# Optimization experiments

Hardware: AMD Instinct MI355X
Metric: run time of the kernel (lower is better)

## Reference

```python
import jax, jax.numpy as jnp
from jax import lax
import numpy as np

B, A, T = 128, 32, 32
HID = 64
DEG = 7
MODES = 25
OUT_FRAMES = 12
NHEAD, DHEAD = 16, 64


def legendre_tmat(out_frames, degree):
    # normalized Legendre basis evaluated at t_n, shape [degree+1, len(t_n)]
    t = np.arange(-6, out_frames + 1, dtype=np.float32)
    t = t / t[-1]
    P = [np.ones_like(t), t]
    for n in range(1, degree):
        P.append(((2 * n + 1) * t * P[n] - n * P[n - 1]) / (n + 1))
    P = np.stack(P[: degree + 1], 0)
    norm = np.sqrt((2 * np.arange(degree + 1) + 1) / 2.0).astype(np.float32)
    return (P * norm[:, None]).astype(np.float32)


def _conv(x, w, stride, pad):
    return lax.conv_general_dilated(x, w, (stride, stride), [(pad, pad), (pad, pad)],
                                    dimension_numbers=("NCHW", "OIHW", "NCHW"))


def _bn(x, g, b, eps=1e-5):
    m = jnp.mean(x, axis=(0, 2, 3), keepdims=True)
    v = jnp.var(x, axis=(0, 2, 3), keepdims=True)
    return (x - m) / jnp.sqrt(v + eps) * g[None, :, None, None] + b[None, :, None, None]


def setup_inputs() -> dict:
    key = jax.random.key(0)
    ks = jax.random.split(key, 32)

    def rn(i, shape, scale=0.05):
        return jax.random.normal(ks[i], shape, dtype=jnp.float32) * scale

    inp = {
        "cnn_feat": rn(0, (B, 1024, 14, 14), 1.0),
        "ego_state": rn(1, (B, T, 5), 1.0),
        "agents_state": rn(2, (B, A, T, 5), 1.0),
        "ego_state_len": jax.random.randint(ks[3], (B,), 0, T),
        "agents_state_len": jax.random.randint(ks[4], (B, A), 0, T),
        "agents_grid_pos": jax.random.randint(ks[5], (B, A, 2), 0, 14),
        "state_fc_W": rn(6, (HID, 5)), "state_fc_b": rn(7, (HID,)),
        "lstm_Wih": rn(8, (4 * HID, HID)), "lstm_Whh": rn(9, (4 * HID, HID)),
        "lstm_bih": rn(10, (4 * HID,)), "lstm_bhh": rn(11, (4 * HID,)),
        "enc_fc_W": rn(12, (HID, HID)), "enc_fc_b": rn(13, (HID,)),
        "conv1_W": rn(14, (512, 1024 + HID, 3, 3)),
        "bn1_g": jnp.ones((512,), jnp.float32), "bn1_b": jnp.zeros((512,), jnp.float32),
        "conv2_W": rn(15, (512, 512, 3, 3)),
        "bn2_g": jnp.ones((512,), jnp.float32), "bn2_b": jnp.zeros((512,), jnp.float32),
        "q_W": rn(16, (NHEAD * DHEAD, 512 + HID)),
        "k_W": rn(17, (NHEAD * DHEAD, 512, 1, 1)),
        "v_W": rn(18, (NHEAD * DHEAD, 512, 1, 1)),
        "attn_out_W": rn(19, (512, NHEAD * DHEAD)), "attn_out_b": rn(20, (512,)),
        "cls_W": rn(21, (MODES, 512 + HID + 512)), "cls_b": rn(22, (MODES,)),
        "dec1_W": rn(23, (256, 512 + HID + 512)), "dec1_b": rn(24, (256,)),
        "dec2_W": rn(25, ((DEG + 1) * 2 * MODES, 256)), "dec2_b": rn(26, ((DEG + 1) * 2 * MODES,)),
    }
    return inp


def reference(cnn_feat, ego_state, agents_state, ego_state_len, agents_state_len,
              agents_grid_pos, state_fc_W, state_fc_b, lstm_Wih, lstm_Whh, lstm_bih,
              lstm_bhh, enc_fc_W, enc_fc_b, conv1_W, bn1_g, bn1_b, conv2_W, bn2_g,
              bn2_b, q_W, k_W, v_W, attn_out_W, attn_out_b, cls_W, cls_b, dec1_W,
              dec1_b, dec2_W, dec2_b):
    Bn, _, Hs, Ws = cnn_feat.shape

    def lstm_encode(seq, lens):
        # seq [N,T,5]; packed-sequence semantics with zero init == take h at step len-1
        N, Tn, _ = seq.shape
        h = seq @ state_fc_W.T + state_fc_b  # [N,T,64]

        def step(carry, xt):
            hh, cc = carry
            g = xt @ lstm_Wih.T + hh @ lstm_Whh.T + lstm_bih + lstm_bhh
            i, f_, gg, o = jnp.split(g, 4, axis=-1)
            cc = jax.nn.sigmoid(f_) * cc + jax.nn.sigmoid(i) * jnp.tanh(gg)
            hh = jax.nn.sigmoid(o) * jnp.tanh(cc)
            return (hh, cc), hh

        z = jnp.zeros((N, HID), h.dtype)
        _, hs = lax.scan(step, (z, z), h.transpose(1, 0, 2))  # hs [T,N,64]
        idx = jnp.clip(lens, 1, Tn).astype(jnp.int32) - 1
        last = hs[idx, jnp.arange(N)]
        return last @ enc_fc_W.T + enc_fc_b

    ego = lstm_encode(ego_state, ego_state_len)  # [B,64]
    ag = lstm_encode(agents_state.reshape(Bn * A, T, 5),
                     agents_state_len.reshape(-1)).reshape(Bn, A, HID)

    # scatter-add agent encodings into the spatial grid (overlapping writes accumulate)
    grid = jnp.zeros((Bn, Hs, Ws, HID), cnn_feat.dtype)
    bidx = jnp.broadcast_to(jnp.arange(Bn)[:, None], (Bn, A))
    grid = grid.at[bidx, agents_grid_pos[..., 0], agents_grid_pos[..., 1]].add(ag)

    x = jnp.concatenate([cnn_feat, grid.transpose(0, 3, 1, 2)], axis=1)
    x = jax.nn.relu(_bn(_conv(x, conv1_W, 1, 1), bn1_g, bn1_b))
    x = jax.nn.relu(_bn(_conv(x, conv2_W, 2, 1), bn2_g, bn2_b))  # [B,512,7,7]

    ego_t = jnp.concatenate([x[:, :, 3, 3], ego], axis=1)  # [B,576]
    q = (ego_t @ q_W.T).reshape(Bn, NHEAD, DHEAD)
    k = _conv(x, k_W, 1, 1).reshape(Bn, NHEAD, DHEAD, -1)  # g = 9*9 = 81
    v = _conv(x, v_W, 1, 1).reshape(Bn, NHEAD, DHEAD, -1)
    energy = jnp.einsum("bhf,bhfg->bhg", q, k)
    attn = jax.nn.softmax(energy / (NHEAD * DHEAD) ** 0.5, axis=2)
    o = jnp.einsum("bhg,bhdg->bhd", attn, v).reshape(Bn, -1)
    o = o @ attn_out_W.T + attn_out_b

    feat = jnp.concatenate([o, ego_t], axis=1)  # [B,1088]
    conf = feat @ cls_W.T + cls_b
    d = jax.nn.relu(feat @ dec1_W.T + dec1_b)
    d = (d @ dec2_W.T + dec2_b).reshape(Bn, MODES, -1)

    tmat = jnp.asarray(legendre_tmat(OUT_FRAMES, DEG))  # [DEG+1, 19]
    out_x = d[:, :, : DEG + 1] @ tmat
    out_y = d[:, :, DEG + 1:] @ tmat
    traj = jnp.stack([out_x, out_y], axis=3)  # [B,MODES,19,2]
    return traj, conf
```

## Files before the change

### kernel.cpp

```cpp
#include <hip/hip_runtime.h>
#include <stdint.h>
#include <stddef.h>

#define DEVINL static __device__ __forceinline__

typedef __attribute__((ext_vector_type(8))) short  bfrag;
typedef __attribute__((ext_vector_type(4))) float  facc;

DEVINL uint16_t f2b(float f){
  uint32_t u = __float_as_uint(f);
  return (uint16_t)((u + 0x7fffu + ((u >> 16) & 1u)) >> 16);
}
DEVINL float b2f(uint16_t b){ return __uint_as_float(((uint32_t)b) << 16); }

DEVINL facc MFMA(bfrag a, bfrag b, facc c){
  return __builtin_amdgcn_mfma_f32_16x16x32_bf16(a, b, c, 0, 0, 0);
}

DEVINL void gload16(const void* g, void* l){
  __builtin_amdgcn_global_load_lds(
      (const __attribute__((address_space(1))) uint32_t*)g,
      (__attribute__((address_space(3))) uint32_t*)l, 16, 0, 0);
}

DEVINL float fast_tanh(float x){
  return 2.f/(1.f+__expf(-2.f*x)) - 1.f;
}

struct F2BJobs {
  const float* s[7];
  uint16_t*    d[7];
  int          n[7];
};
__global__ void k_f2b_multi(F2BJobs jobs){
  int j = blockIdx.y;
  const float* s = jobs.s[j];
  uint16_t* d = jobs.d[j];
  int n = jobs.n[j];
  int i = blockIdx.x*256 + threadIdx.x;
  int st = gridDim.x*256;
  for(; i<n; i+=st) d[i] = f2b(s[i]);
}

__global__ void k_zborder(uint16_t* __restrict__ X, int C){
  int b = blockIdx.x, t = threadIdx.x;
  for(int p=0;p<60;p++){
    int y, x;
    if(p<16){ y=0; x=p; }
    else if(p<32){ y=15; x=p-16; }
    else { int q=p-32; y=1+(q>>1); x=(q&1)?15:0; }
    uint32_t* dst = (uint32_t*)(X + ((size_t)(b*16+y)*16 + x)*C);
    for(int i=t;i<C/2;i+=256) dst[i] = 0;
  }
}

__global__ void k_lstm_prep(const float* __restrict__ Wih, const float* __restrict__ Whh,
                            const float* __restrict__ bih, const float* __restrict__ bhh,
                            const float* __restrict__ sW, const float* __restrict__ sb,
                            const float* __restrict__ encW,
                            uint16_t* __restrict__ Wc, float* __restrict__ be,
                            uint16_t* __restrict__ encWb, float* __restrict__ tm){
  int n = threadIdx.x;
  if(n < 19){
    float tv = (float)(n - 6) / 12.0f;
    float Pm = 1.0f, Pc = tv;
    tm[0*19+n] = Pm * sqrtf(0.5f);
    tm[1*19+n] = Pc * sqrtf(1.5f);
    for(int q=1; q<7; q++){
      float Pn = ((float)(2*q+1)*tv*Pc - (float)q*Pm) / (float)(q+1);
      Pm = Pc; Pc = Pn;
      tm[(q+1)*19+n] = Pc * sqrtf((float)(2*(q+1)+1) * 0.5f);
    }
  }
  for(int k=0;k<64;k++) Wc[n*96+k] = f2b(Whh[n*64+k]);
  for(int k5=0;k5<5;k5++){
    float s = 0.f;
    for(int j=0;j<64;j++) s += Wih[n*64+j]*sW[j*5+k5];
    Wc[n*96+64+k5] = f2b(s);
  }
  for(int k=69;k<96;k++) Wc[n*96+k] = 0;
  float s = 0.f;
  for(int j=0;j<64;j++) s += Wih[n*64+j]*sb[j];
  be[n] = s + bih[n] + bhh[n];
  if(n < 64){
    for(int k=0;k<64;k++) encWb[n*64+k] = f2b(encW[n*64+k]);
  }
}

__global__ __launch_bounds__(256) void k_lstm(
    const float* __restrict__ ego_seq, const float* __restrict__ ag_seq,
    const int* __restrict__ ego_len, const int* __restrict__ ag_len,
    const int* __restrict__ grid_pos,
    const uint16_t* __restrict__ Wc, const float* __restrict__ be,
    const uint16_t* __restrict__ encWb, const float* __restrict__ encB,
    float* __restrict__ agrid, uint16_t* __restrict__ egoT, uint16_t* __restrict__ feat)
{
  __shared__ __align__(16) uint16_t A[32*96];
  __shared__ float Xf[32*160];
  __shared__ int   idxs[32];

  int t = threadIdx.x, w = t>>6, l = t&63;
  int blk = blockIdx.x;
  bool isEgo = blk < 4;
  int seq0 = isEgo ? blk*32 : (blk-4)*32;
  const float* seqp = (isEgo ? ego_seq : ag_seq) + (size_t)seq0*160;

  for(int i=t;i<32*160;i+=256) Xf[i] = seqp[i];
  if(t < 32){
    int L = isEgo ? ego_len[seq0+t] : ag_len[seq0+t];
    if(L < 1) L = 1;
    idxs[t] = L-1;
  }
  for(int i=t;i<32*96;i+=256) A[i] = 0;

  bfrag bf[4][3];
  float be4[4];
  for(int ct=0;ct<4;ct++){
    int n = (ct*4+w)*16 + (l&15);
    for(int ks=0;ks<3;ks++)
      bf[ct][ks] = *(const bfrag*)(Wc + n*96 + ks*32 + (l>>4)*8);
    be4[ct] = be[n];
  }
  float cst[8], hl[8];
  for(int i=0;i<8;i++){ cst[i]=0.f; hl[i]=0.f; }
  __syncthreads();
  int myidx[8];
  for(int rt=0;rt<2;rt++) for(int r=0;r<4;r++){
    int s = rt*16 + (l>>4)*4 + r;
    myidx[rt*4+r] = idxs[s];
  }

  for(int st=0; st<32; st++){
    if(t < 160){ int s=t/5, kk=t%5; A[s*96+64+kk] = f2b(Xf[s*160 + st*5 + kk]); }
    __syncthreads();
    facc acc[2][4];
    for(int rt=0;rt<2;rt++) for(int ct=0;ct<4;ct++) acc[rt][ct] = facc{0.f,0.f,0.f,0.f};
    #pragma unroll
    for(int ks=0;ks<3;ks++){
      bfrag aA[2];
      #pragma unroll
      for(int rt=0;rt<2;rt++)
        aA[rt] = *(const bfrag*)(A + (rt*16+(l&15))*96 + ks*32 + (l>>4)*8);
      #pragma unroll
      for(int rt=0;rt<2;rt++)
        #pragma unroll
        for(int ct=0;ct<4;ct++)
          acc[rt][ct] = MFMA(aA[rt], bf[ct][ks], acc[rt][ct]);
    }
    __syncthreads();
    #pragma unroll
    for(int rt=0;rt<2;rt++) for(int r=0;r<4;r++){
      int cell = rt*4+r;
      int s = rt*16 + (l>>4)*4 + r;
      float gi = acc[rt][0][r] + be4[0];
      float gf = acc[rt][1][r] + be4[1];
      float gg = acc[rt][2][r] + be4[2];
      float go = acc[rt][3][r] + be4[3];
      float si = 1.f/(1.f+__expf(-gi));
      float sf = 1.f/(1.f+__expf(-gf));
      float so = 1.f/(1.f+__expf(-go));
      float tg = fast_tanh(gg);
      float c2 = sf*cst[cell] + si*tg;
      cst[cell] = c2;
      float hn = so*fast_tanh(c2);
      A[s*96 + w*16 + (l&15)] = f2b(hn);
      if(st == myidx[cell]) hl[cell] = hn;
    }
  }
  __syncthreads();
  for(int rt=0;rt<2;rt++) for(int r=0;r<4;r++){
    int s = rt*16 + (l>>4)*4 + r;
    A[s*96 + w*16 + (l&15)] = f2b(hl[rt*4+r]);
  }
  __syncthreads();
  bfrag eb[2];
  for(int ks=0;ks<2;ks++)
    eb[ks] = *(const bfrag*)(encWb + (w*16+(l&15))*64 + ks*32 + (l>>4)*8);
  facc ea[2]; ea[0] = facc{0.f,0.f,0.f,0.f}; ea[1] = facc{0.f,0.f,0.f,0.f};
  for(int ks=0;ks<2;ks++){
    for(int rt=0;rt<2;rt++){
      bfrag aA = *(const bfrag*)(A + (rt*16+(l&15))*96 + ks*32 + (l>>4)*8);
      ea[rt] = MFMA(aA, eb[ks], ea[rt]);
    }
  }
  int n = w*16 + (l&15);
  float bn_ = encB[n];
  for(int rt=0;rt<2;rt++) for(int r=0;r<4;r++){
    int s = rt*16 + (l>>4)*4 + r;
    float v = ea[rt][r] + bn_;
    int gs = seq0 + s;
    if(isEgo){
      egoT[(size_t)gs*576 + 512 + n] = f2b(v);
      feat[(size_t)gs*1088 + 1024 + n] = f2b(v);
    } else {
      int py = grid_pos[gs*2+0], px = grid_pos[gs*2+1];
      atomicAdd(&agrid[((size_t)(gs>>5)*196 + py*14 + px)*64 + n], v);
    }
  }
}

__global__ void k_packx(const float* __restrict__ cnn, const float* __restrict__ agrid,
                        uint16_t* __restrict__ Xp)
{
  __shared__ float tile[32*200];
  int b = blockIdx.x, ch = blockIdx.y, t = threadIdx.x;
  if(ch < 32){
    int c0 = ch*32;
    for(int i=t;i<32*196;i+=256){
      int ci = i/196, s = i%196;
      tile[ci*200+s] = cnn[((size_t)b*1024 + c0+ci)*196 + s];
    }
    __syncthreads();
    for(int i=t;i<32*196;i+=256){
      int s = i>>5, ci = i&31;
      int y = s/14, x = s%14;
      Xp[(((size_t)b*16 + y+1)*16 + x+1)*1088 + c0 + ci] = f2b(tile[ci*200+s]);
    }
  } else {
    int j0 = (ch-32)*32;
    for(int i=t;i<32*196;i+=256){
      int s = i>>5, ji = i&31;
      int y = s/14, x = s%14;
      Xp[(((size_t)b*16 + y+1)*16 + x+1)*1088 + 1024 + j0 + ji] =
          f2b(agrid[((size_t)b*196 + s)*64 + j0 + ji]);
    }
  }
}

__global__ void k_packw(const float* __restrict__ W, uint16_t* __restrict__ Wp, int O, int C)
{
  int o = blockIdx.x;
  int c = blockIdx.y*64 + threadIdx.x;
  const float* src = W + ((size_t)o*C + c)*9;
  float v[9];
  #pragma unroll
  for(int d=0;d<9;d++) v[d] = src[d];
  #pragma unroll
  for(int d=0;d<9;d++)
    Wp[((size_t)d*O + o)*C + c] = f2b(v[d]);
}

__global__ __launch_bounds__(512) void k_conv1_8p(
    const uint16_t* __restrict__ Ain, const uint16_t* __restrict__ Wb,
    uint16_t* __restrict__ Out, float* __restrict__ stats)
{
  constexpr int CB = 1088;
  constexpr int NSTEP = 153;
  __shared__ __align__(16) char LDSb[131072];

  int t = threadIdx.x, w = t>>6, l = t&63;
  int wm = w>>2, wn = w&3;

  int xcd = blockIdx.x & 7, pos = blockIdx.x >> 3;
  int wgid = (xcd < 4 ? xcd*25 : 100 + (xcd-4)*24) + pos;
  int m0 = (wgid % 98) * 256;
  int n0 = (wgid / 98) * 256;

  const uint16_t* aP[2][2];
  const uint16_t* bP[2][2];
  #pragma unroll
  for(int P=0;P<2;P++)
    #pragma unroll
    for(int j=0;j<2;j++){
      int partrow = j*64 + (t>>3);
      int swz = ((t&7) ^ (partrow&7))*8;
      int gr = P*64 + partrow + ((partrow>=64)?64:0);
      int m = m0 + gr; int b = m/196, s = m%196, y = s/14, x = s%14;
      aP[P][j] = Ain + ((b*16+y)*16+x)*CB + swz;
      int nb = n0 + (partrow>>5)*64 + P*32 + (partrow&31);
      bP[P][j] = Wb + (size_t)nb*CB + swz;
    }

  facc acc[8][4];
  #pragma unroll
  for(int i=0;i<8;i++)
    #pragma unroll
    for(int j=0;j<4;j++) acc[i][j] = facc{0.f,0.f,0.f,0.f};

  int dd = 0;

  #define STG(buf, PART) do{                                                   \
    if((PART)==0 || (PART)==3){ const int P_ = ((PART)==3);                    \
      _Pragma("unroll")                                                        \
      for(int j_=0;j_<2;j_++)                                                  \
        gload16(aP[P_][j_], LDSb + (buf)*65536 + P_*16384 + j_*8192 + w*1024); \
    } else { const int P_ = ((PART)==2);                                       \
      _Pragma("unroll")                                                        \
      for(int j_=0;j_<2;j_++)                                                  \
        gload16(bP[P_][j_], LDSb + (buf)*65536 + 32768 + P_*16384 + j_*8192 + w*1024); \
    }                                                                          \
  }while(0)

  #define ADVK() do{                                                          \
    if(dd==8){                                                                \
      _Pragma("unroll")                                                       \
      for(int P_=0;P_<2;P_++) for(int j_=0;j_<2;j_++){                        \
        aP[P_][j_] += 64 - 34*CB; bP[P_][j_] += 64 - 8*512*CB; }              \
      dd = 0;                                                                 \
    } else {                                                                  \
      int sA_ = (dd==2||dd==5) ? 14*CB : CB;                                  \
      _Pragma("unroll")                                                       \
      for(int P_=0;P_<2;P_++) for(int j_=0;j_<2;j_++){                        \
        aP[P_][j_] += sA_; bP[P_][j_] += 512*CB; }                            \
      dd++;                                                                   \
    }                                                                         \
  }while(0)

  #define VM4 asm volatile("s_waitcnt vmcnt(4)" ::: "memory")
  #define VM2 asm volatile("s_waitcnt vmcnt(2)" ::: "memory")
  #define VM0 asm volatile("s_waitcnt vmcnt(0)" ::: "memory")

  #define PHASE(mh, nh, SP, DO_STG, WAIT) do{                                 \
    const uint16_t* Ab_ = (const uint16_t*)(LDSb + p*65536 + (mh)*16384);     \
    const uint16_t* Bb_ = (const uint16_t*)(LDSb + p*65536 + 32768 + (nh)*16384); \
    bfrag a_[4][2], b_[2][2];                                                 \
    _Pragma("unroll")                                                         \
    for(int i_=0;i_<4;i_++)                                                   \
      _Pragma("unroll")                                                       \
      for(int ks_=0;ks_<2;ks_++)                                              \
        a_[i_][ks_] = *(const bfrag*)(Ab_ + (wm*64 + i_*16 + (l&15))*64       \
                        + ((ks_*32 + (l>>4)*8) ^ ((l&7)<<3)));                \
    _Pragma("unroll")                                                         \
    for(int j_=0;j_<2;j_++)                                                   \
      _Pragma("unroll")                                                       \
      for(int ks_=0;ks_<2;ks_++)                                              \
        b_[j_][ks_] = *(const bfrag*)(Bb_ + (wn*32 + j_*16 + (l&15))*64       \
                        + ((ks_*32 + (l>>4)*8) ^ ((l&7)<<3)));                \
    if(DO_STG) STG(p^1, SP);                                                  \
    __builtin_amdgcn_sched_barrier(0);                                        \
    __builtin_amdgcn_s_barrier();                                             \
    __builtin_amdgcn_s_setprio(1);                                            \
    _Pragma("unroll")                                                         \
    for(int ks_=0;ks_<2;ks_++)                                                \
      _Pragma("unroll")                                                       \
      for(int i_=0;i_<4;i_++)                                                 \
        _Pragma("unroll")                                                     \
        for(int j_=0;j_<2;j_++)                                               \
          acc[(mh)*4+i_][(nh)*2+j_] =                                         \
            MFMA(a_[i_][ks_], b_[j_][ks_], acc[(mh)*4+i_][(nh)*2+j_]);        \
    __builtin_amdgcn_s_setprio(0);                                            \
    WAIT;                                                                     \
    __builtin_amdgcn_s_barrier();                                             \
  }while(0)

  STG(0,0); STG(0,1); STG(0,2); STG(0,3);
  ADVK();
  VM4;
  __builtin_amdgcn_s_barrier();

  for(int kt=0; kt<NSTEP-1; kt++){
    int p = kt&1;
    PHASE(0,0, 0, 1, VM4);
    PHASE(0,1, 1, 1, VM4);
    PHASE(1,0, 2, 1, (void)0);
    PHASE(1,1, 3, 1, VM4);
    if(kt < NSTEP-2) ADVK();
  }
  {
    int p = 0;
    PHASE(0,0, 0, 0, VM2);
    PHASE(0,1, 1, 0, VM0);
    PHASE(1,0, 2, 0, (void)0);
    PHASE(1,1, 3, 0, (void)0);
  }

  #undef PHASE
  #undef STG
  #undef ADVK

  __syncthreads();
  int* oo = (int*)LDSb;
  if(t < 256){
    int m = m0 + t; int b = m/196, s = m%196, y = s/14, x = s%14;
    oo[t] = ((b*16 + y+1)*16 + (x+1))*512;
  }
  __syncthreads();
  #pragma unroll
  for(int i=0;i<8;i++)
    #pragma unroll
    for(int j=0;j<4;j++){
      int n = n0 + wn*64 + j*16 + (l&15);
      #pragma unroll
      for(int r=0;r<4;r++){
        int mr = wm*128 + i*16 + (l>>4)*4 + r;
        Out[(size_t)oo[mr] + n] = f2b(acc[i][j][r]);
      }
    }
  __syncthreads();
  float* sred = (float*)LDSb;
  int rg = wm*4 + (l>>4);
  #pragma unroll
  for(int j=0;j<4;j++){
    float s=0.f, q=0.f;
    #pragma unroll
    for(int i=0;i<8;i++)
      #pragma unroll
      for(int r=0;r<4;r++){ float v = acc[i][j][r]; s += v; q += v*v; }
    int nl = wn*64 + j*16 + (l&15);
    sred[(nl*8 + rg)*2+0] = s;
    sred[(nl*8 + rg)*2+1] = q;
  }
  __syncthreads();
  if(t < 256){
    float s=0.f, q=0.f;
    #pragma unroll
    for(int rgi=0;rgi<8;rgi++){ s += sred[(t*8+rgi)*2]; q += sred[(t*8+rgi)*2+1]; }
    atomicAdd(&stats[n0+t], s);
    atomicAdd(&stats[512+n0+t], q);
  }
}

template<int MODE>
__global__ __launch_bounds__(256) void k_conv(
    const uint16_t* __restrict__ Ain, const uint16_t* __restrict__ Wb,
    uint16_t* __restrict__ Out, float* __restrict__ stats)
{
  constexpr int CB   = 512;
  constexpr int NB   = (MODE==2) ? 2048 : 512;
  constexpr int NDY  = (MODE==2) ? 1 : 9;
  constexpr int NCC  = 8;
  constexpr int MT   = 49;
  constexpr int NT   = NB/128;
  constexpr int NWG  = MT*NT;
  constexpr int Q8   = NWG/8, R8 = NWG%8;

  __shared__ __align__(16) uint16_t As[128*64];
  __shared__ __align__(16) uint16_t Bs[128*64];
  __shared__ int outOff[128];

  int t = threadIdx.x, w = t>>6, l = t&63;

  int xcd = blockIdx.x & 7, pos = blockIdx.x >> 3;
  int wgid = (xcd < R8 ? xcd*(Q8+1) : R8*(Q8+1) + (xcd-R8)*Q8) + pos;
  int n0 = (wgid / MT) * 128;
  int m0 = (wgid % MT) * 128;

  if(t < 128){
    int m = m0 + t;
    outOff[t] = (MODE==1) ? m*512 : m*2048;
  }

  const uint16_t* aP[4];
  const uint16_t* bP[4];
  #pragma unroll
  for(int p=0;p<4;p++){
    int r = w*32 + p*8 + (l>>3);
    int m = m0 + r, ro;
    if(MODE==1){
      int b = m/49, s = m%49, y = s/7, x = s%7;
      ro = ((b*16 + 2*y)*16 + 2*x)*512;
    } else {
      ro = m*512;
    }
    aP[p] = Ain + ro + (l&7)*8;
    bP[p] = Wb + (size_t)(n0 + r)*CB + (l&7)*8;
  }
  __syncthreads();

  facc acc[4][4];
  #pragma unroll
  for(int i=0;i<4;i++)
    #pragma unroll
    for(int j=0;j<4;j++) acc[i][j] = facc{0.f,0.f,0.f,0.f};
  int wm = w>>1, wn = w&1;
  char* asDst = (char*)As + w*4096;
  char* bsDst = (char*)Bs + w*4096;

  for(int cc=0; cc<NCC; cc++){
    for(int d=0; d<NDY; d++){
      #pragma unroll
      for(int p=0;p<4;p++) gload16(aP[p], asDst + p*1024);
      #pragma unroll
      for(int p=0;p<4;p++) gload16(bP[p], bsDst + p*1024);
      if(MODE != 2){
        int stepA = ((d%3)==2) ? 14*CB : CB;
        #pragma unroll
        for(int p=0;p<4;p++){ aP[p] += stepA; bP[p] += NB*CB; }
      }
      __syncthreads();
      #pragma unroll
      for(int ks=0;ks<2;ks++){
        bfrag a[4], b[4];
        #pragma unroll
        for(int i=0;i<4;i++)
          a[i] = *(const bfrag*)(As + (wm*64 + i*16 + (l&15))*64 + ks*32 + (l>>4)*8);
        #pragma unroll
        for(int j=0;j<4;j++)
          b[j] = *(const bfrag*)(Bs + (wn*64 + j*16 + (l&15))*64 + ks*32 + (l>>4)*8);
        #pragma unroll
        for(int i=0;i<4;i++)
          #pragma unroll
          for(int j=0;j<4;j++)
            acc[i][j] = MFMA(a[i], b[j], acc[i][j]);
      }
      __syncthreads();
    }
    int resetA = (MODE==2) ? 64 : 64 - 48*CB;
    int resetB = (MODE==2) ? 64 : 64 - 9*NB*CB;
    #pragma unroll
    for(int p=0;p<4;p++){ aP[p] += resetA; bP[p] += resetB; }
  }

  #pragma unroll
  for(int i=0;i<4;i++)
    #pragma unroll
    for(int j=0;j<4;j++){
      int n = n0 + wn*64 + j*16 + (l&15);
      #pragma unroll
      for(int r=0;r<4;r++){
        int mr = wm*64 + i*16 + (l>>4)*4 + r;
        Out[(size_t)outOff[mr] + n] = f2b(acc[i][j][r]);
      }
    }

  if(MODE != 2){
    __syncthreads();
    float* sred = (float*)As;
    int rg = wm*4 + (l>>4);
    #pragma unroll
    for(int j=0;j<4;j++){
      float s=0.f, q=0.f;
      #pragma unroll
      for(int i=0;i<4;i++)
        #pragma unroll
        for(int r=0;r<4;r++){ float v = acc[i][j][r]; s += v; q += v*v; }
      int nl = wn*64 + j*16 + (l&15);
      sred[(nl*8 + rg)*2+0] = s;
      sred[(nl*8 + rg)*2+1] = q;
    }
    __syncthreads();
    if(t < 128){
      float s=0.f, q=0.f;
      #pragma unroll
      for(int rgi=0;rgi<8;rgi++){ s += sred[(t*8+rgi)*2]; q += sred[(t*8+rgi)*2+1]; }
      atomicAdd(&stats[n0+t], s);
      atomicAdd(&stats[512+n0+t], q);
    }
  }
}

template<int PAD>
__global__ void k_bnapply(uint16_t* __restrict__ Y, const float* __restrict__ stats,
                          const float* __restrict__ gg, const float* __restrict__ bb,
                          int M, float invM,
                          uint16_t* __restrict__ egoT, uint16_t* __restrict__ feat)
{
  int t = threadIdx.x;
  int m0 = blockIdx.x*8;
  float mu0 = stats[2*t]*invM,       mu1 = stats[2*t+1]*invM;
  float v0 = stats[512+2*t]*invM - mu0*mu0, v1 = stats[512+2*t+1]*invM - mu1*mu1;
  float sc0 = gg[2*t]  *rsqrtf(v0+1e-5f), sc1 = gg[2*t+1]*rsqrtf(v1+1e-5f);
  float sh0 = bb[2*t]   - mu0*sc0,        sh1 = bb[2*t+1] - mu1*sc1;
  for(int i=0;i<8;i++){
    int m = m0+i; if(m>=M) break;
    size_t off;
    if(PAD){ int b=m/196, s=m%196, y=s/14, x=s%14; off = (((size_t)b*16+y+1)*16 + x+1)*512; }
    else off = (size_t)m*512;
    uint32_t u = *(const uint32_t*)(Y + off + 2*t);
    float a = fmaxf(b2f((uint16_t)u)*sc0 + sh0, 0.f);
    float c = fmaxf(b2f((uint16_t)(u>>16))*sc1 + sh1, 0.f);
    uint32_t pu = (uint32_t)f2b(a) | ((uint32_t)f2b(c)<<16);
    *(uint32_t*)(Y + off + 2*t) = pu;
    if(!PAD && (m%49)==24){
      int b = m/49;
      *(uint32_t*)(egoT + (size_t)b*576 + 2*t) = pu;
      *(uint32_t*)(feat + (size_t)b*1088 + 512 + 2*t) = pu;
    }
  }
}

__global__ __launch_bounds__(256) void k_sgemm(
    const uint16_t* __restrict__ A, int lda,
    const uint16_t* __restrict__ B, int ldb,
    const float* __restrict__ bias,
    void* __restrict__ C, int ldc,
    int N, int K, int flags)
{
  int t = threadIdx.x, w = t>>6, l = t&63;
  int nt = blockIdx.x*4 + w;
  int n  = nt*16 + (l&15);
  int m0 = blockIdx.y*16;
  bool nv = n < N;
  facc acc = facc{0.f,0.f,0.f,0.f};
  for(int k=0;k<K;k+=32){
    bfrag af = *(const bfrag*)(A + (size_t)(m0+(l&15))*lda + k + (l>>4)*8);
    bfrag bf_ = {0,0,0,0,0,0,0,0};
    if(nv) bf_ = *(const bfrag*)(B + (size_t)n*ldb + k + (l>>4)*8);
    acc = MFMA(af, bf_, acc);
  }
  if(nv){
    float bv = bias ? bias[n] : 0.f;
    #pragma unroll
    for(int r=0;r<4;r++){
      int m = m0 + (l>>4)*4 + r;
      float v = acc[r] + bv;
      if(flags & 1) v = fmaxf(v, 0.f);
      if(flags & 2) ((float*)C)[(size_t)m*ldc + n] = v;
      else ((uint16_t*)C)[(size_t)m*ldc + n] = f2b(v);
    }
  }
}

__global__ __launch_bounds__(256) void k_attn(
    const float* __restrict__ q, const uint16_t* __restrict__ kv,
    uint16_t* __restrict__ o)
{
  int t = threadIdx.x, w = t>>6, l = t&63;
  int idx = blockIdx.x*4 + w;
  int b = idx>>4, h = idx&15;
  float qf = q[(size_t)b*1024 + h*64 + l];
  const uint16_t* kp = kv + (size_t)b*49*2048 + h*64 + l;
  float eo = 0.f;
  for(int g=0; g<49; g++){
    float p = qf * b2f(kp[(size_t)g*2048]);
    for(int s=32;s>0;s>>=1) p += __shfl_xor(p, s);
    if(l == g) eo = p;
  }
  float e = (l<49) ? eo*(1.f/32.f) : -1e30f;
  float mx = e;
  for(int s=32;s>0;s>>=1) mx = fmaxf(mx, __shfl_xor(mx, s));
  mx = fmaxf(mx, 0.f);
  float p = (l<49) ? __expf(e-mx) : 0.f;
  float den = p;
  for(int s=32;s>0;s>>=1) den += __shfl_xor(den, s);
  den += 32.f*__expf(-mx);
  const uint16_t* vp = kv + (size_t)b*49*2048 + 1024 + h*64 + l;
  float accv = 0.f;
  for(int g=0; g<49; g++){
    float pg = __shfl(p, g);
    accv += pg * b2f(vp[(size_t)g*2048]);
  }
  o[(size_t)b*1024 + h*64 + l] = f2b(accv/den);
}

__global__ void k_traj(const float* __restrict__ d2, const float* __restrict__ tm,
                       float* __restrict__ out)
{
  int i = blockIdx.x*256 + threadIdx.x;
  if(i >= 3200) return;
  const float* dp = d2 + (size_t)i*16;
  float cx[8], cy[8];
  #pragma unroll
  for(int j=0;j<8;j++){ cx[j]=dp[j]; cy[j]=dp[8+j]; }
  float* op = out + (size_t)i*38;
  for(int tt=0;tt<19;tt++){
    float x=0.f, y=0.f;
    #pragma unroll
    for(int j=0;j<8;j++){ float tv = tm[j*19+tt]; x += cx[j]*tv; y += cy[j]*tv; }
    op[tt*2+0]=x; op[tt*2+1]=y;
  }
}

extern "C" void kernel_launch(void* const* d_in, const int* in_sizes, int n_in,
                              void* d_out, int out_size, void* d_ws, size_t ws_size,
                              hipStream_t stream)
{
  const float* cnn      = (const float*)d_in[0];
  const float* ego_seq  = (const float*)d_in[1];
  const float* ag_seq   = (const float*)d_in[2];
  const int*   ego_len  = (const int*)d_in[3];
  const int*   ag_len   = (const int*)d_in[4];
  const int*   grid_pos = (const int*)d_in[5];
  const float* sW  = (const float*)d_in[6];
  const float* sb  = (const float*)d_in[7];
  const float* Wih = (const float*)d_in[8];
  const float* Whh = (const float*)d_in[9];
  const float* bih = (const float*)d_in[10];
  const float* bhh = (const float*)d_in[11];
  const float* encW = (const float*)d_in[12];
  const float* encB = (const float*)d_in[13];
  const float* conv1W = (const float*)d_in[14];
  const float* bn1g = (const float*)d_in[15];
  const float* bn1b = (const float*)d_in[16];
  const float* conv2W = (const float*)d_in[17];
  const float* bn2g = (const float*)d_in[18];
  const float* bn2b = (const float*)d_in[19];
  const float* qWf  = (const float*)d_in[20];
  const float* kWf  = (const float*)d_in[21];
  const float* vWf  = (const float*)d_in[22];
  const float* aoW  = (const float*)d_in[23];
  const float* aoB  = (const float*)d_in[24];
  const float* clsWf = (const float*)d_in[25];
  const float* clsB  = (const float*)d_in[26];
  const float* d1Wf  = (const float*)d_in[27];
  const float* d1B   = (const float*)d_in[28];
  const float* d2Wf  = (const float*)d_in[29];
  const float* d2B   = (const float*)d_in[30];

  char* ws = (char*)d_ws;
  const size_t XP_OFF   = 0;
  const size_t KV_OFF   = 0;
  const size_t Y2_OFF   = 29360128;
  const size_t Y1P_OFF  = 71303168;
  const size_t WP1_OFF  = 104857600;
  const size_t WP2_OFF  = 114884608;
  const size_t WKV_OFF  = 119603200;
  const size_t QW_OFF   = 121700352;
  const size_t AOW_OFF  = 122880000;
  const size_t CLSW_OFF = 123928576;
  const size_t D1W_OFF  = 123982976;
  const size_t D2W_OFF  = 124540032;
  const size_t GRID_OFF = 124744832;
  const size_t EGOT_OFF = 131167360;
  const size_t FEAT_OFF = 131314816;
  const size_t QBUF_OFF = 131593344;
  const size_t OBUF_OFF = 132117632;
  const size_t D1_OFF   = 132379776;
  const size_t D2_OFF   = 132445312;
  const size_t WC_OFF   = 132650112;
  const size_t BE_OFF   = 132699264;
  const size_t ENCW_OFF = 132700288;
  const size_t TMAT_OFF = 132708480;
  const size_t ST1_OFF  = 132709120;
  const size_t ST2_OFF  = 132713216;

  uint16_t* XP   = (uint16_t*)(ws + XP_OFF);
  uint16_t* KV   = (uint16_t*)(ws + KV_OFF);
  uint16_t* Y2   = (uint16_t*)(ws + Y2_OFF);
  uint16_t* Y1P  = (uint16_t*)(ws + Y1P_OFF);
  uint16_t* WP1  = (uint16_t*)(ws + WP1_OFF);
  uint16_t* WP2  = (uint16_t*)(ws + WP2_OFF);
  uint16_t* WKV  = (uint16_t*)(ws + WKV_OFF);
  uint16_t* QW   = (uint16_t*)(ws + QW_OFF);
  uint16_t* AOW  = (uint16_t*)(ws + AOW_OFF);
  uint16_t* CLSW = (uint16_t*)(ws + CLSW_OFF);
  uint16_t* D1W  = (uint16_t*)(ws + D1W_OFF);
  uint16_t* D2W  = (uint16_t*)(ws + D2W_OFF);
  float*    GRIDB= (float*)(ws + GRID_OFF);
  uint16_t* EGOT = (uint16_t*)(ws + EGOT_OFF);
  uint16_t* FEAT = (uint16_t*)(ws + FEAT_OFF);
  float*    QBUF = (float*)(ws + QBUF_OFF);
  uint16_t* OBUF = (uint16_t*)(ws + OBUF_OFF);
  uint16_t* D1B  = (uint16_t*)(ws + D1_OFF);
  float*    D2B  = (float*)(ws + D2_OFF);
  uint16_t* WC   = (uint16_t*)(ws + WC_OFF);
  float*    BE   = (float*)(ws + BE_OFF);
  uint16_t* ENCWB= (uint16_t*)(ws + ENCW_OFF);
  float*    TMAT = (float*)(ws + TMAT_OFF);
  float*    ST1  = (float*)(ws + ST1_OFF);
  float*    ST2  = (float*)(ws + ST2_OFF);
  float*    outF = (float*)d_out;

  (void)hipMemsetAsync(ws + GRID_OFF, 0, 6422528, stream);
  (void)hipMemsetAsync(ws + ST1_OFF,  0, 8192, stream);

  k_zborder<<<128,256,0,stream>>>(XP, 1088);
  k_zborder<<<128,256,0,stream>>>(Y1P, 512);

  k_lstm_prep<<<1,256,0,stream>>>(Wih,Whh,bih,bhh,sW,sb,encW, WC,BE,ENCWB, TMAT);
  k_packw<<<dim3(512,17),64,0,stream>>>(conv1W, WP1, 512, 1088);
  k_packw<<<dim3(512,8), 64,0,stream>>>(conv2W, WP2, 512, 512);
  {
    F2BJobs jb;
    jb.s[0]=kWf;  jb.d[0]=WKV;              jb.n[0]=1024*512;
    jb.s[1]=vWf;  jb.d[1]=WKV + 1024*512;   jb.n[1]=1024*512;
    jb.s[2]=qWf;  jb.d[2]=QW;               jb.n[2]=1024*576;
    jb.s[3]=aoW;  jb.d[3]=AOW;              jb.n[3]=512*1024;
    jb.s[4]=clsWf;jb.d[4]=CLSW;             jb.n[4]=25*1088;
    jb.s[5]=d1Wf; jb.d[5]=D1W;              jb.n[5]=256*1088;
    jb.s[6]=d2Wf; jb.d[6]=D2W;              jb.n[6]=400*256;
    k_f2b_multi<<<dim3(48,7),256,0,stream>>>(jb);
  }

  k_lstm<<<132,256,0,stream>>>(ego_seq, ag_seq, ego_len, ag_len, grid_pos,
                               WC, BE, ENCWB, encB, GRIDB, EGOT, FEAT);
  k_packx<<<dim3(128,34),256,0,stream>>>(cnn, GRIDB, XP);
  k_conv1_8p<<<196,512,0,stream>>>(XP, WP1, Y1P, ST1);
  k_bnapply<1><<<3136,256,0,stream>>>(Y1P, ST1, bn1g, bn1b, 25088, 1.f/25088.f, nullptr, nullptr);
  k_conv<1><<<196,256,0,stream>>>(Y1P, WP2, Y2, ST2);
  k_bnapply<0><<<784,256,0,stream>>>(Y2, ST2, bn2g, bn2b, 6272, 1.f/6272.f, EGOT, FEAT);
  k_conv<2><<<784,256,0,stream>>>(Y2, WKV, KV, nullptr);
  k_sgemm<<<dim3(16,8),256,0,stream>>>(EGOT, 576, QW, 576, nullptr, QBUF, 1024, 1024, 576, 2);
  k_attn<<<512,256,0,stream>>>(QBUF, KV, OBUF);
  k_sgemm<<<dim3(8,8),256,0,stream>>>(OBUF, 1024, AOW, 1024, aoB, FEAT, 1088, 512, 1024, 0);
  k_sgemm<<<dim3(1,8),256,0,stream>>>(FEAT, 1088, CLSW, 1088, clsB, outF + 121600, 25, 25, 1088, 2);
  k_sgemm<<<dim3(4,8),256,0,stream>>>(FEAT, 1088, D1W, 1088, d1B, D1B, 256, 256, 1088, 1);
  k_sgemm<<<dim3(7,8),256,0,stream>>>(D1B, 256, D2W, 256, d2B, D2B, 400, 400, 256, 2);
  k_traj<<<13,256,0,stream>>>(D2B, TMAT, outF);

  (void)in_sizes; (void)n_in; (void)out_size; (void)ws_size;
}
```

Measured before the change: 677.0 us.

## Split conv2 over kernel rows into fp32 partials, reduce with BN stats

The stride-2 conv2 is split along its kernel-row dimension (dy) across a second grid axis, so each workgroup covers one row of three taps over a 1536-long K. This triples the workgroup count from 196 to 588 to fill more CUs. It adds a separate reduction kernel that sums the three fp32 partial planes, writes bf16 Y2 and accumulates BN statistics. The conv2 weights are repacked into a per-dy contiguous layout, the two border-zeroing launches are merged into one, and the KV 1x1 conv becomes its own specialized kernel. The cost is extra global traffic for roughly 38 MB of fp32 partials plus one more launch.

New measurement: 664.3 us. Within noise of the previous version (-1.9%).

```diff
diff --git a/kernel.cpp b/kernel.cpp
--- a/kernel.cpp
+++ b/kernel.cpp
@@ -42,14 +42,16 @@
   for(; i<n; i+=st) d[i] = f2b(s[i]);
 }
 
-__global__ void k_zborder(uint16_t* __restrict__ X, int C){
-  int b = blockIdx.x, t = threadIdx.x;
+__global__ void k_zborder(uint16_t* __restrict__ X, uint16_t* __restrict__ Y){
+  int b = blockIdx.x & 127, t = threadIdx.x;
+  uint16_t* base = (blockIdx.x < 128) ? X : Y;
+  int C = (blockIdx.x < 128) ? 1088 : 512;
   for(int p=0;p<60;p++){
     int y, x;
     if(p<16){ y=0; x=p; }
     else if(p<32){ y=15; x=p-16; }
     else { int q=p-32; y=1+(q>>1); x=(q&1)?15:0; }
-    uint32_t* dst = (uint32_t*)(X + ((size_t)(b*16+y)*16 + x)*C);
+    uint32_t* dst = (uint32_t*)(base + ((size_t)(b*16+y)*16 + x)*C);
     for(int i=t;i<C/2;i+=256) dst[i] = 0;
   }
 }
@@ -238,6 +240,21 @@
   #pragma unroll
   for(int d=0;d<9;d++)
     Wp[((size_t)d*O + o)*C + c] = f2b(v[d]);
+}
+
+__global__ void k_packw2(const float* __restrict__ W, uint16_t* __restrict__ Wp)
+{
+  int o = blockIdx.x;
+  int c = blockIdx.y*64 + threadIdx.x;
+  const float* src = W + ((size_t)o*512 + c)*9;
+  float v[9];
+  #pragma unroll
+  for(int d=0;d<9;d++) v[d] = src[d];
+  #pragma unroll
+  for(int dy=0;dy<3;dy++)
+    #pragma unroll
+    for(int dx=0;dx<3;dx++)
+      Wp[((size_t)(dy*512 + o))*1536 + dx*512 + c] = f2b(v[dy*3+dx]);
 }
 
 __global__ __launch_bounds__(512) void k_conv1_8p(
@@ -410,52 +427,31 @@
   }
 }
 
-template<int MODE>
-__global__ __launch_bounds__(256) void k_conv(
+__global__ __launch_bounds__(256) void k_conv2dy(
     const uint16_t* __restrict__ Ain, const uint16_t* __restrict__ Wb,
-    uint16_t* __restrict__ Out, float* __restrict__ stats)
-{
-  constexpr int CB   = 512;
-  constexpr int NB   = (MODE==2) ? 2048 : 512;
-  constexpr int NDY  = (MODE==2) ? 1 : 9;
-  constexpr int NCC  = 8;
-  constexpr int MT   = 49;
-  constexpr int NT   = NB/128;
-  constexpr int NWG  = MT*NT;
-  constexpr int Q8   = NWG/8, R8 = NWG%8;
-
+    float* __restrict__ PS)
+{
   __shared__ __align__(16) uint16_t As[128*64];
   __shared__ __align__(16) uint16_t Bs[128*64];
-  __shared__ int outOff[128];
 
   int t = threadIdx.x, w = t>>6, l = t&63;
+  int dy = blockIdx.y;
 
   int xcd = blockIdx.x & 7, pos = blockIdx.x >> 3;
-  int wgid = (xcd < R8 ? xcd*(Q8+1) : R8*(Q8+1) + (xcd-R8)*Q8) + pos;
-  int n0 = (wgid / MT) * 128;
-  int m0 = (wgid % MT) * 128;
-
-  if(t < 128){
-    int m = m0 + t;
-    outOff[t] = (MODE==1) ? m*512 : m*2048;
-  }
+  int wgid = (xcd < 4 ? xcd*25 : 100 + (xcd-4)*24) + pos;
+  int n0 = (wgid / 49) * 128;
+  int m0 = (wgid % 49) * 128;
 
   const uint16_t* aP[4];
   const uint16_t* bP[4];
   #pragma unroll
   for(int p=0;p<4;p++){
     int r = w*32 + p*8 + (l>>3);
-    int m = m0 + r, ro;
-    if(MODE==1){
-      int b = m/49, s = m%49, y = s/7, x = s%7;
-      ro = ((b*16 + 2*y)*16 + 2*x)*512;
-    } else {
-      ro = m*512;
-    }
-    aP[p] = Ain + ro + (l&7)*8;
-    bP[p] = Wb + (size_t)(n0 + r)*CB + (l&7)*8;
-  }
-  __syncthreads();
+    int m = m0 + r;
+    int b = m/49, s = m%49, y = s/7, x = s%7;
+    aP[p] = Ain + ((b*16 + 2*y + dy)*16 + 2*x)*512 + (l&7)*8;
+    bP[p] = Wb + ((size_t)(dy*512 + n0 + r))*1536 + (l&7)*8;
+  }
 
   facc acc[4][4];
   #pragma unroll
@@ -466,41 +462,31 @@
   char* asDst = (char*)As + w*4096;
   char* bsDst = (char*)Bs + w*4096;
 
-  for(int cc=0; cc<NCC; cc++){
-    for(int d=0; d<NDY; d++){
-      #pragma unroll
-      for(int p=0;p<4;p++) gload16(aP[p], asDst + p*1024);
-      #pragma unroll
-      for(int p=0;p<4;p++) gload16(bP[p], bsDst + p*1024);
-      if(MODE != 2){
-        int stepA = ((d%3)==2) ? 14*CB : CB;
-        #pragma unroll
-        for(int p=0;p<4;p++){ aP[p] += stepA; bP[p] += NB*CB; }
-      }
-      __syncthreads();
-      #pragma unroll
-      for(int ks=0;ks<2;ks++){
-        bfrag a[4], b[4];
-        #pragma unroll
-        for(int i=0;i<4;i++)
-          a[i] = *(const bfrag*)(As + (wm*64 + i*16 + (l&15))*64 + ks*32 + (l>>4)*8);
+  for(int stp=0; stp<24; stp++){
+    #pragma unroll
+    for(int p=0;p<4;p++){ gload16(aP[p], asDst + p*1024); aP[p] += 64; }
+    #pragma unroll
+    for(int p=0;p<4;p++){ gload16(bP[p], bsDst + p*1024); bP[p] += 64; }
+    __syncthreads();
+    #pragma unroll
+    for(int ks=0;ks<2;ks++){
+      bfrag a[4], b[4];
+      #pragma unroll
+      for(int i=0;i<4;i++)
+        a[i] = *(const bfrag*)(As + (wm*64 + i*16 + (l&15))*64 + ks*32 + (l>>4)*8);
+      #pragma unroll
+      for(int j=0;j<4;j++)
+        b[j] = *(const bfrag*)(Bs + (wn*64 + j*16 + (l&15))*64 + ks*32 + (l>>4)*8);
+      #pragma unroll
+      for(int i=0;i<4;i++)
         #pragma unroll
         for(int j=0;j<4;j++)
-          b[j] = *(const bfrag*)(Bs + (wn*64 + j*16 + (l&15))*64 + ks*32 + (l>>4)*8);
-        #pragma unroll
-        for(int i=0;i<4;i++)
-          #pragma unroll
-          for(int j=0;j<4;j++)
-            acc[i][j] = MFMA(a[i], b[j], acc[i][j]);
-      }
-      __syncthreads();
-    }
-    int resetA = (MODE==2) ? 64 : 64 - 48*CB;
-    int resetB = (MODE==2) ? 64 : 64 - 9*NB*CB;
-    #pragma unroll
-    for(int p=0;p<4;p++){ aP[p] += resetA; bP[p] += resetB; }
-  }
-
+          acc[i][j] = MFMA(a[i], b[j], acc[i][j]);
+    }
+    __syncthreads();
+  }
+
+  float* out = PS + (size_t)dy*3211264;
   #pragma unroll
   for(int i=0;i<4;i++)
     #pragma unroll
@@ -508,35 +494,105 @@
       int n = n0 + wn*64 + j*16 + (l&15);
       #pragma unroll
       for(int r=0;r<4;r++){
-        int mr = wm*64 + i*16 + (l>>4)*4 + r;
-        Out[(size_t)outOff[mr] + n] = f2b(acc[i][j][r]);
+        int mr = m0 + wm*64 + i*16 + (l>>4)*4 + r;
+        out[(size_t)mr*512 + n] = acc[i][j][r];
       }
     }
-
-  if(MODE != 2){
+}
+
+__global__ void k_bn2sum(const float* __restrict__ PS, uint16_t* __restrict__ Y2,
+                         float* __restrict__ stats)
+{
+  int t = threadIdx.x;
+  int m0 = blockIdx.x*128;
+  float s0=0,s1=0,q0=0,q1=0;
+  for(int i=0;i<128;i++){
+    size_t off = (size_t)(m0+i)*512 + 2*t;
+    float2 p0 = *(const float2*)(PS + off);
+    float2 p1 = *(const float2*)(PS + 3211264 + off);
+    float2 p2 = *(const float2*)(PS + 6422528 + off);
+    float a = p0.x+p1.x+p2.x, c = p0.y+p1.y+p2.y;
+    s0+=a; q0+=a*a; s1+=c; q1+=c*c;
+    *(uint32_t*)(Y2 + off) = (uint32_t)f2b(a) | ((uint32_t)f2b(c)<<16);
+  }
+  atomicAdd(&stats[2*t],   s0);
+  atomicAdd(&stats[2*t+1], s1);
+  atomicAdd(&stats[512+2*t],   q0);
+  atomicAdd(&stats[512+2*t+1], q1);
+}
+
+__global__ __launch_bounds__(256) void k_convkv(
+    const uint16_t* __restrict__ Ain, const uint16_t* __restrict__ Wb,
+    uint16_t* __restrict__ Out)
+{
+  constexpr int CB = 512;
+  constexpr int NB = 2048;
+  constexpr int NWG = 49*16;
+  constexpr int Q8 = NWG/8;
+
+  __shared__ __align__(16) uint16_t As[128*64];
+  __shared__ __align__(16) uint16_t Bs[128*64];
+
+  int t = threadIdx.x, w = t>>6, l = t&63;
+
+  int xcd = blockIdx.x & 7, pos = blockIdx.x >> 3;
+  int wgid = xcd*Q8 + pos;
+  int n0 = (wgid / 49) * 128;
+  int m0 = (wgid % 49) * 128;
+
+  const uint16_t* aP[4];
+  const uint16_t* bP[4];
+  #pragma unroll
+  for(int p=0;p<4;p++){
+    int r = w*32 + p*8 + (l>>3);
+    aP[p] = Ain + (size_t)(m0 + r)*512 + (l&7)*8;
+    bP[p] = Wb + (size_t)(n0 + r)*CB + (l&7)*8;
+  }
+
+  facc acc[4][4];
+  #pragma unroll
+  for(int i=0;i<4;i++)
+    #pragma unroll
+    for(int j=0;j<4;j++) acc[i][j] = facc{0.f,0.f,0.f,0.f};
+  int wm = w>>1, wn = w&1;
+  char* asDst = (char*)As + w*4096;
+  char* bsDst = (char*)Bs + w*4096;
+
+  for(int cc=0; cc<8; cc++){
+    #pragma unroll
+    for(int p=0;p<4;p++){ gload16(aP[p], asDst + p*1024); aP[p] += 64; }
+    #pragma unroll
+    for(int p=0;p<4;p++){ gload16(bP[p], bsDst + p*1024); bP[p] += 64; }
     __syncthreads();
-    float* sred = (float*)As;
-    int rg = wm*4 + (l>>4);
-    #pragma unroll
-    for(int j=0;j<4;j++){
-      float s=0.f, q=0.f;
+    #pragma unroll
+    for(int ks=0;ks<2;ks++){
+      bfrag a[4], b[4];
+      #pragma unroll
+      for(int i=0;i<4;i++)
+        a[i] = *(const bfrag*)(As + (wm*64 + i*16 + (l&15))*64 + ks*32 + (l>>4)*8);
+      #pragma unroll
+      for(int j=0;j<4;j++)
+        b[j] = *(const bfrag*)(Bs + (wn*64 + j*16 + (l&15))*64 + ks*32 + (l>>4)*8);
       #pragma unroll
       for(int i=0;i<4;i++)
         #pragma unroll
-        for(int r=0;r<4;r++){ float v = acc[i][j][r]; s += v; q += v*v; }
-      int nl = wn*64 + j*16 + (l&15);
-      sred[(nl*8 + rg)*2+0] = s;
-      sred[(nl*8 + rg)*2+1] = q;
+        for(int j=0;j<4;j++)
+          acc[i][j] = MFMA(a[i], b[j], acc[i][j]);
     }
     __syncthreads();
-    if(t < 128){
-      float s=0.f, q=0.f;
-      #pragma unroll
-      for(int rgi=0;rgi<8;rgi++){ s += sred[(t*8+rgi)*2]; q += sred[(t*8+rgi)*2+1]; }
-      atomicAdd(&stats[n0+t], s);
-      atomicAdd(&stats[512+n0+t], q);
-    }
-  }
+  }
+
+  #pragma unroll
+  for(int i=0;i<4;i++)
+    #pragma unroll
+    for(int j=0;j<4;j++){
+      int n = n0 + wn*64 + j*16 + (l&15);
+      #pragma unroll
+      for(int r=0;r<4;r++){
+        int mr = m0 + wm*64 + i*16 + (l>>4)*4 + r;
+        Out[(size_t)mr*2048 + n] = f2b(acc[i][j][r]);
+      }
+    }
 }
 
 template<int PAD>
@@ -689,8 +745,9 @@
 
   char* ws = (char*)d_ws;
   const size_t XP_OFF   = 0;
+  const size_t PS_OFF   = 0;
   const size_t KV_OFF   = 0;
-  const size_t Y2_OFF   = 29360128;
+  const size_t Y2_OFF   = 41943040;
   const size_t Y1P_OFF  = 71303168;
   const size_t WP1_OFF  = 104857600;
   const size_t WP2_OFF  = 114884608;
@@ -715,6 +772,7 @@
   const size_t ST2_OFF  = 132713216;
 
   uint16_t* XP   = (uint16_t*)(ws + XP_OFF);
+  float*    PS   = (float*)(ws + PS_OFF);
   uint16_t* KV   = (uint16_t*)(ws + KV_OFF);
   uint16_t* Y2   = (uint16_t*)(ws + Y2_OFF);
   uint16_t* Y1P  = (uint16_t*)(ws + Y1P_OFF);
@@ -744,12 +802,11 @@
   (void)hipMemsetAsync(ws + GRID_OFF, 0, 6422528, stream);
   (void)hipMemsetAsync(ws + ST1_OFF,  0, 8192, stream);
 
-  k_zborder<<<128,256,0,stream>>>(XP, 1088);
-  k_zborder<<<128,256,0,stream>>>(Y1P, 512);
+  k_zborder<<<256,256,0,stream>>>(XP, Y1P);
 
   k_lstm_prep<<<1,256,0,stream>>>(Wih,Whh,bih,bhh,sW,sb,encW, WC,BE,ENCWB, TMAT);
   k_packw<<<dim3(512,17),64,0,stream>>>(conv1W, WP1, 512, 1088);
-  k_packw<<<dim3(512,8), 64,0,stream>>>(conv2W, WP2, 512, 512);
+  k_packw2<<<dim3(512,8),64,0,stream>>>(conv2W, WP2);
   {
     F2BJobs jb;
     jb.s[0]=kWf;  jb.d[0]=WKV;              jb.n[0]=1024*512;
@@ -767,9 +824,10 @@
   k_packx<<<dim3(128,34),256,0,stream>>>(cnn, GRIDB, XP);
   k_conv1_8p<<<196,512,0,stream>>>(XP, WP1, Y1P, ST1);
   k_bnapply<1><<<3136,256,0,stream>>>(Y1P, ST1, bn1g, bn1b, 25088, 1.f/25088.f, nullptr, nullptr);
-  k_conv<1><<<196,256,0,stream>>>(Y1P, WP2, Y2, ST2);
+  k_conv2dy<<<dim3(196,3),256,0,stream>>>(Y1P, WP2, PS);
+  k_bn2sum<<<49,256,0,stream>>>(PS, Y2, ST2);
   k_bnapply<0><<<784,256,0,stream>>>(Y2, ST2, bn2g, bn2b, 6272, 1.f/6272.f, EGOT, FEAT);
-  k_conv<2><<<784,256,0,stream>>>(Y2, WKV, KV, nullptr);
+  k_convkv<<<784,256,0,stream>>>(Y2, WKV, KV);
   k_sgemm<<<dim3(16,8),256,0,stream>>>(EGOT, 576, QW, 576, nullptr, QBUF, 1024, 1024, 576, 2);
   k_attn<<<512,256,0,stream>>>(QBUF, KV, OBUF);
   k_sgemm<<<dim3(8,8),256,0,stream>>>(OBUF, 1024, AOW, 1024, aoB, FEAT, 1088, 512, 1024, 0);
```
